# Optimization experiments

Measured on AMD Instinct MI355X. Metric: run time of the kernel, lower is better.

## Reference

```python
import jax, jax.numpy as jnp
import numpy as np
from jax import lax

TOP_K = 8
N_EXPERTS = 256
N_GROUP = 8
TOPK_GROUP = 4
ROUTED_SCALING = 2.5
NORM_TOPK_PROB = True


def setup_inputs() -> dict:
    key = jax.random.key(0)
    k1, k2, k3 = jax.random.split(key, 3)
    hidden_states = jax.random.normal(k1, (4, 4096, 4096), dtype=jnp.float32)
    weight = jax.random.normal(k2, (N_EXPERTS, 4096), dtype=jnp.float32) * 0.02
    e_score_correction_bias = jax.random.normal(k3, (N_EXPERTS,), dtype=jnp.float32) * 0.1
    return {
        "hidden_states": hidden_states,
        "weight": weight,
        "e_score_correction_bias": e_score_correction_bias,
    }


def reference(hidden_states, weight, e_score_correction_bias):
    bsz, seq_len, h = hidden_states.shape
    T = bsz * seq_len
    x = hidden_states.reshape(T, h).astype(jnp.float32)
    # gate GEMM: [T, h] x [E, h]^T -> [T, E]
    logits = jnp.einsum("th,eh->te", x, weight.astype(jnp.float32))
    scores = jax.nn.sigmoid(logits)

    scores_for_choice = scores + e_score_correction_bias[None, :]  # [T, E]
    eg = N_EXPERTS // N_GROUP  # experts per group
    grp = scores_for_choice.reshape(T, N_GROUP, eg)
    top2, _ = lax.top_k(grp, 2)                      # [T, G, 2]
    group_scores = top2.sum(axis=-1)                  # [T, G]
    _, group_idx = lax.top_k(group_scores, TOPK_GROUP)  # [T, topk_group]
    group_mask = jnp.zeros((T, N_GROUP), dtype=scores.dtype)
    group_mask = group_mask.at[jnp.arange(T)[:, None], group_idx].set(1.0)
    score_mask = jnp.broadcast_to(group_mask[:, :, None], (T, N_GROUP, eg)).reshape(T, N_EXPERTS)

    neg_inf = jnp.float32(-jnp.inf)
    tmp_scores = jnp.where(score_mask > 0, scores_for_choice, neg_inf)
    _, topk_idx = lax.top_k(tmp_scores, TOP_K)        # [T, top_k]
    topk_weight = jnp.take_along_axis(scores, topk_idx, axis=1)

    if TOP_K > 1 and NORM_TOPK_PROB:
        denom = topk_weight.sum(axis=-1, keepdims=True) + 1e-20
        topk_weight = topk_weight / denom
    topk_weight = topk_weight * ROUTED_SCALING
    return topk_idx, topk_weight
```

## Files before the change

### kernel.cpp

```cpp
#include <hip/hip_runtime.h>
#include <math.h>

#define Hdim 4096
#define NE 256
#define BM 64
#define BK 32
#define NKC (Hdim / BK)
#define PLANE_ELEMS (Hdim * NE)
#define CHUNK_ELEMS 8192

#define C0 9.765625e-4f
#define C1 4.76837158203125e-7f

typedef _Float16 f16x8 __attribute__((ext_vector_type(8)));
typedef _Float16 f16x4 __attribute__((ext_vector_type(4)));
typedef float f32x4 __attribute__((ext_vector_type(4)));

#define KBAR()                                               \
  {                                                          \
    asm volatile("s_waitcnt lgkmcnt(0)" ::: "memory");       \
    __builtin_amdgcn_s_barrier();                            \
  }

__global__ __launch_bounds__(256)
void convert_w(const float* __restrict__ W, _Float16* __restrict__ pl) {
  const int id = blockIdx.x * 256 + threadIdx.x;
  const int k8 = id & 511;
  const int n = id >> 9;
  const float* src = W + (long)n * Hdim + k8 * 8;
  const float4 x0 = *(const float4*)src;
  const float4 x1 = *(const float4*)(src + 4);
  const float xv[8] = {x0.x, x0.y, x0.z, x0.w, x1.x, x1.y, x1.z, x1.w};
  f16x8 vh, vm;
#pragma unroll
  for (int j = 0; j < 8; ++j) {
    const float v = xv[j] * 64.f;
    const _Float16 h = (_Float16)v;
    const float r = (v - (float)h) * 2048.f;
    vh[j] = h;
    vm[j] = (_Float16)r;
  }
  const long co = ((long)k8 * NE + n) * 8;
  *(f16x8*)(pl + co) = vh;
  *(f16x8*)(pl + PLANE_ELEMS + co) = vm;
}

__global__ __launch_bounds__(512, 2)
void moe_gate_fused(const float* __restrict__ X, const _Float16* __restrict__ pl,
                    const float* __restrict__ bias, float* __restrict__ out, int T) {
  __shared__ __align__(16) unsigned char smem[66560];
  const int tid = threadIdx.x;
  const int lane = tid & 63, wave = tid >> 6;
  const int r16 = lane & 15, c4 = lane >> 4;
  const long bm0 = (long)blockIdx.x * BM;

  f32x4 acc0[4][2], acc1[4][2];
#pragma unroll
  for (int i = 0; i < 4; ++i)
#pragma unroll
    for (int j = 0; j < 2; ++j) {
      acc0[i][j] = (f32x4)(0.f);
      acc1[i][j] = (f32x4)(0.f);
    }

  const int xm = tid >> 3;
  const int f4 = tid & 7;
  const float* xsrc = X + (bm0 + xm) * (long)Hdim + f4 * 4;
  const int k8w = f4 >> 1, hw = f4 & 1;
  const int xws = k8w * 1024 + xm * 16 + hw * 8;

  const _Float16* wsrc0 = pl + ((size_t)(c4 * 256 + wave * 32 + r16)) * 8;
  const _Float16* wsrc1 = wsrc0 + PLANE_ELEMS;

  f16x8 wA[2][2][2], wB[2][2][2];

#define LOADW(dst, pair_)                                                       \
  {                                                                             \
    _Pragma("unroll") for (int sc = 0; sc < 2; ++sc) {                          \
      const size_t ko = (size_t)((pair_) * 2 + sc) * CHUNK_ELEMS;               \
      _Pragma("unroll") for (int fn = 0; fn < 2; ++fn) {                        \
        dst[sc][0][fn] = *(const f16x8*)(wsrc0 + ko + fn * 128);                \
        dst[sc][1][fn] = *(const f16x8*)(wsrc1 + ko + fn * 128);                \
      }                                                                         \
    }                                                                           \
  }

#define LOADX(pair_)                                                            \
  {                                                                             \
    xn0 = *(const float4*)(xsrc + (size_t)(pair_) * 64);                        \
    xn1 = *(const float4*)(xsrc + (size_t)(pair_) * 64 + 32);                   \
  }

#define WRITE_X2(b, xr0, xr1)                                                   \
  {                                                                             \
    _Pragma("unroll") for (int sc = 0; sc < 2; ++sc) {                          \
      const float4 xr = sc ? (xr1) : (xr0);                                     \
      f16x4 vh, vm;                                                             \
      const float xa[4] = {xr.x, xr.y, xr.z, xr.w};                             \
      _Pragma("unroll") for (int j = 0; j < 4; ++j) {                           \
        const float v = xa[j] * 16.f;                                           \
        const _Float16 h = (_Float16)v;                                         \
        const float r = (v - (float)h) * 2048.f;                                \
        vh[j] = h;                                                              \
        vm[j] = (_Float16)r;                                                    \
      }                                                                         \
      const int xo = (b) * 16384 + sc * 8192 + xws;                             \
      *(f16x4*)&smem[xo] = vh;                                                  \
      *(f16x4*)&smem[xo + 4096] = vm;                                           \
    }                                                                           \
  }

#define COMPUTE(b, sc, wreg)                                                    \
  {                                                                             \
    const int xo = (b) * 16384 + (sc) * 8192;                                   \
    f16x8 af[2][4];                                                             \
    _Pragma("unroll") for (int p = 0; p < 2; ++p)                               \
        _Pragma("unroll") for (int fm = 0; fm < 4; ++fm)                        \
            af[p][fm] = *(const f16x8*)&smem[xo + p * 4096 + c4 * 1024 +        \
                                             (fm * 16 + r16) * 16];             \
    _Pragma("unroll") for (int fm = 0; fm < 4; ++fm)                            \
        _Pragma("unroll") for (int fn = 0; fn < 2; ++fn) {                      \
      acc0[fm][fn] = __builtin_amdgcn_mfma_f32_16x16x32_f16(                    \
          af[0][fm], wreg[sc][0][fn], acc0[fm][fn], 0, 0, 0);                   \
      f32x4 s = acc1[fm][fn];                                                   \
      s = __builtin_amdgcn_mfma_f32_16x16x32_f16(af[0][fm], wreg[sc][1][fn], s, 0, 0, 0); \
      s = __builtin_amdgcn_mfma_f32_16x16x32_f16(af[1][fm], wreg[sc][0][fn], s, 0, 0, 0); \
      acc1[fm][fn] = s;                                                         \
    }                                                                           \
  }

  float4 xn0, xn1;

  LOADX(0);
  WRITE_X2(0, xn0, xn1);
  LOADW(wA, 0);
  __syncthreads();

  for (int p = 0; p < NKC / 2; p += 2) {
    {
      LOADX(p + 1);
      LOADW(wB, p + 1);
      __builtin_amdgcn_sched_barrier(0);
      COMPUTE(0, 0, wA);
      COMPUTE(0, 1, wA);
      WRITE_X2(1, xn0, xn1);
      KBAR();
    }
    {
      const int pn = (p + 2 < NKC / 2) ? p + 2 : NKC / 2 - 1;
      LOADX(pn);
      LOADW(wA, pn);
      __builtin_amdgcn_sched_barrier(0);
      COMPUTE(1, 0, wB);
      COMPUTE(1, 1, wB);
      if (p + 2 < NKC / 2) WRITE_X2(0, xn0, xn1);
      KBAR();
    }
  }

  __syncthreads();
  float* lg = (float*)smem;
#pragma unroll
  for (int fm = 0; fm < 4; ++fm)
#pragma unroll
    for (int fn = 0; fn < 2; ++fn)
#pragma unroll
      for (int r = 0; r < 4; ++r) {
        const int t = fm * 16 + c4 * 4 + r;
        const int n = wave * 32 + fn * 16 + r16;
        lg[t * 260 + n] = fmaf(acc1[fm][fn][r], C1, acc0[fm][fn][r] * C0);
      }
  __syncthreads();

  const float4 bv = *(const float4*)(bias + lane * 4);
  for (int i = 0; i < 8; ++i) {
    const int t = wave * 8 + i;
    const float4 lgv = *(const float4*)&lg[t * 260 + lane * 4];

    const float s0 = 1.f / (1.f + expf(-lgv.x));
    const float s1 = 1.f / (1.f + expf(-lgv.y));
    const float s2 = 1.f / (1.f + expf(-lgv.z));
    const float s3 = 1.f / (1.f + expf(-lgv.w));

    const float c0 = s0 + bv.x, c1 = s1 + bv.y, c2 = s2 + bv.z, c3 = s3 + bv.w;

    float m1 = fmaxf(c0, c1), m2 = fminf(c0, c1);
    if (c2 > m1) { m2 = m1; m1 = c2; } else m2 = fmaxf(m2, c2);
    if (c3 > m1) { m2 = m1; m1 = c3; } else m2 = fmaxf(m2, c3);
#pragma unroll
    for (int off = 1; off < 8; off <<= 1) {
      const float o1 = __shfl_xor(m1, off);
      const float o2 = __shfl_xor(m2, off);
      if (o1 > m1) { m2 = fmaxf(m1, o2); m1 = o1; }
      else m2 = fmaxf(m2, o1);
    }
    const float gs = m1 + m2;

    const int gme = lane >> 3;
    int rank = 0;
#pragma unroll
    for (int j = 0; j < 8; ++j) {
      const float gj = __shfl(gs, j * 8);
      rank += ((gj > gs) || (gj == gs && j < gme)) ? 1 : 0;
    }
    const bool sel = rank < 4;

    const float NEG = -INFINITY;
    float q0 = sel ? c0 : NEG, q1 = sel ? c1 : NEG;
    float q2 = sel ? c2 : NEG, q3 = sel ? c3 : NEG;

    float sum = 0.f;
    int my_e = 0;
    float my_w = 0.f;
#pragma unroll
    for (int r = 0; r < 8; ++r) {
      float v = q0; int ix = 0;
      if (q1 > v) { v = q1; ix = 1; }
      if (q2 > v) { v = q2; ix = 2; }
      if (q3 > v) { v = q3; ix = 3; }
      int e = lane * 4 + ix;
#pragma unroll
      for (int off = 1; off < 64; off <<= 1) {
        const float v2 = __shfl_xor(v, off);
        const int e2 = __shfl_xor(e, off);
        const bool take = (v2 > v) || (v2 == v && e2 < e);
        v = take ? v2 : v;
        e = take ? e2 : e;
      }
      const int slot = e & 3, owner = e >> 2;
      const float svs = (slot == 0) ? s0 : ((slot == 1) ? s1 : ((slot == 2) ? s2 : s3));
      const float wgt = __shfl(svs, owner);
      sum += wgt;
      if (lane == r) { my_e = e; my_w = wgt; }
      const bool own = (lane == owner);
      q0 = (own && slot == 0) ? NEG : q0;
      q1 = (own && slot == 1) ? NEG : q1;
      q2 = (own && slot == 2) ? NEG : q2;
      q3 = (own && slot == 3) ? NEG : q3;
    }

    if (lane < 8) {
      const float denom = sum + 1e-20f;
      const long tg = bm0 + t;
      out[tg * 8 + lane] = (float)my_e;
      out[(long)T * 8 + tg * 8 + lane] = my_w / denom * 2.5f;
    }
  }
}

extern "C" void kernel_launch(void* const* d_in, const int* in_sizes, int n_in,
                              void* d_out, int out_size, void* d_ws, size_t ws_size,
                              hipStream_t stream) {
  const float* X = (const float*)d_in[0];
  const float* W = (const float*)d_in[1];
  const float* B = (const float*)d_in[2];
  float* out = (float*)d_out;
  const int T = in_sizes[0] / Hdim;

  _Float16* planes = (_Float16*)d_ws;

  convert_w<<<512, 256, 0, stream>>>(W, planes);
  moe_gate_fused<<<T / BM, 512, 0, stream>>>(X, planes, B, out, T);
}
```

Measured before the change: 155.3 us.

## Split gate GEMM along K into two halves with atomic logit accumulation

The fused GEMM+top-k kernel is split in three: a memset of a logits buffer, a GEMM kernel where each of 512 blocks handles one 64-token tile over half of the K dimension and atomically adds partial logits to global memory, and a separate top-k kernel with one wave per token. This doubles the grid from 256 to 512 blocks to fill more CUs, and shrinks LDS use so occupancy can rise. In exchange it adds a 16 MB logits round trip through global memory, float atomics (order-dependent rounding) and two extra launches.

```diff
diff --git a/kernel.cpp b/kernel.cpp
--- a/kernel.cpp
+++ b/kernel.cpp
@@ -46,13 +46,15 @@
 }
 
 __global__ __launch_bounds__(512, 2)
-void moe_gate_fused(const float* __restrict__ X, const _Float16* __restrict__ pl,
-                    const float* __restrict__ bias, float* __restrict__ out, int T) {
-  __shared__ __align__(16) unsigned char smem[66560];
+void gemm_half(const float* __restrict__ X, const _Float16* __restrict__ pl,
+               float* __restrict__ logits) {
+  __shared__ __align__(16) unsigned char smem[32768];
   const int tid = threadIdx.x;
   const int lane = tid & 63, wave = tid >> 6;
   const int r16 = lane & 15, c4 = lane >> 4;
-  const long bm0 = (long)blockIdx.x * BM;
+  const int tile = blockIdx.x & 255;
+  const int p0 = (blockIdx.x >> 8) * 32;
+  const long bm0 = (long)tile * BM;
 
   f32x4 acc0[4][2], acc1[4][2];
 #pragma unroll
@@ -131,12 +133,12 @@
 
   float4 xn0, xn1;
 
-  LOADX(0);
+  LOADX(p0);
   WRITE_X2(0, xn0, xn1);
-  LOADW(wA, 0);
+  LOADW(wA, p0);
   __syncthreads();
 
-  for (int p = 0; p < NKC / 2; p += 2) {
+  for (int p = p0; p < p0 + 32; p += 2) {
     {
       LOADX(p + 1);
       LOADW(wB, p + 1);
@@ -147,19 +149,17 @@
       KBAR();
     }
     {
-      const int pn = (p + 2 < NKC / 2) ? p + 2 : NKC / 2 - 1;
+      const int pn = (p + 2 < p0 + 32) ? p + 2 : p0 + 31;
       LOADX(pn);
       LOADW(wA, pn);
       __builtin_amdgcn_sched_barrier(0);
       COMPUTE(1, 0, wB);
       COMPUTE(1, 1, wB);
-      if (p + 2 < NKC / 2) WRITE_X2(0, xn0, xn1);
+      if (p + 2 < p0 + 32) WRITE_X2(0, xn0, xn1);
       KBAR();
     }
   }
 
-  __syncthreads();
-  float* lg = (float*)smem;
 #pragma unroll
   for (int fm = 0; fm < 4; ++fm)
 #pragma unroll
@@ -168,83 +168,88 @@
       for (int r = 0; r < 4; ++r) {
         const int t = fm * 16 + c4 * 4 + r;
         const int n = wave * 32 + fn * 16 + r16;
-        lg[t * 260 + n] = fmaf(acc1[fm][fn][r], C1, acc0[fm][fn][r] * C0);
+        atomicAdd(&logits[(bm0 + t) * (long)NE + n],
+                  fmaf(acc1[fm][fn][r], C1, acc0[fm][fn][r] * C0));
       }
-  __syncthreads();
-
+}
+
+__global__ __launch_bounds__(256)
+void moe_gate_topk(const float* __restrict__ logits, const float* __restrict__ bias,
+                   float* __restrict__ out, int T) {
+  const int tid = threadIdx.x;
+  const int lane = tid & 63;
+  const int wv_ = tid >> 6;
+  const int t = blockIdx.x * 4 + wv_;
+
+  const float4 lg = *(const float4*)(logits + (long)t * NE + lane * 4);
   const float4 bv = *(const float4*)(bias + lane * 4);
-  for (int i = 0; i < 8; ++i) {
-    const int t = wave * 8 + i;
-    const float4 lgv = *(const float4*)&lg[t * 260 + lane * 4];
-
-    const float s0 = 1.f / (1.f + expf(-lgv.x));
-    const float s1 = 1.f / (1.f + expf(-lgv.y));
-    const float s2 = 1.f / (1.f + expf(-lgv.z));
-    const float s3 = 1.f / (1.f + expf(-lgv.w));
-
-    const float c0 = s0 + bv.x, c1 = s1 + bv.y, c2 = s2 + bv.z, c3 = s3 + bv.w;
-
-    float m1 = fmaxf(c0, c1), m2 = fminf(c0, c1);
-    if (c2 > m1) { m2 = m1; m1 = c2; } else m2 = fmaxf(m2, c2);
-    if (c3 > m1) { m2 = m1; m1 = c3; } else m2 = fmaxf(m2, c3);
-#pragma unroll
-    for (int off = 1; off < 8; off <<= 1) {
-      const float o1 = __shfl_xor(m1, off);
-      const float o2 = __shfl_xor(m2, off);
-      if (o1 > m1) { m2 = fmaxf(m1, o2); m1 = o1; }
-      else m2 = fmaxf(m2, o1);
-    }
-    const float gs = m1 + m2;
-
-    const int gme = lane >> 3;
-    int rank = 0;
-#pragma unroll
-    for (int j = 0; j < 8; ++j) {
-      const float gj = __shfl(gs, j * 8);
-      rank += ((gj > gs) || (gj == gs && j < gme)) ? 1 : 0;
-    }
-    const bool sel = rank < 4;
-
-    const float NEG = -INFINITY;
-    float q0 = sel ? c0 : NEG, q1 = sel ? c1 : NEG;
-    float q2 = sel ? c2 : NEG, q3 = sel ? c3 : NEG;
-
-    float sum = 0.f;
-    int my_e = 0;
-    float my_w = 0.f;
-#pragma unroll
-    for (int r = 0; r < 8; ++r) {
-      float v = q0; int ix = 0;
-      if (q1 > v) { v = q1; ix = 1; }
-      if (q2 > v) { v = q2; ix = 2; }
-      if (q3 > v) { v = q3; ix = 3; }
-      int e = lane * 4 + ix;
-#pragma unroll
-      for (int off = 1; off < 64; off <<= 1) {
-        const float v2 = __shfl_xor(v, off);
-        const int e2 = __shfl_xor(e, off);
-        const bool take = (v2 > v) || (v2 == v && e2 < e);
-        v = take ? v2 : v;
-        e = take ? e2 : e;
-      }
-      const int slot = e & 3, owner = e >> 2;
-      const float svs = (slot == 0) ? s0 : ((slot == 1) ? s1 : ((slot == 2) ? s2 : s3));
-      const float wgt = __shfl(svs, owner);
-      sum += wgt;
-      if (lane == r) { my_e = e; my_w = wgt; }
-      const bool own = (lane == owner);
-      q0 = (own && slot == 0) ? NEG : q0;
-      q1 = (own && slot == 1) ? NEG : q1;
-      q2 = (own && slot == 2) ? NEG : q2;
-      q3 = (own && slot == 3) ? NEG : q3;
-    }
-
-    if (lane < 8) {
-      const float denom = sum + 1e-20f;
-      const long tg = bm0 + t;
-      out[tg * 8 + lane] = (float)my_e;
-      out[(long)T * 8 + tg * 8 + lane] = my_w / denom * 2.5f;
-    }
+
+  const float s0 = 1.f / (1.f + expf(-lg.x));
+  const float s1 = 1.f / (1.f + expf(-lg.y));
+  const float s2 = 1.f / (1.f + expf(-lg.z));
+  const float s3 = 1.f / (1.f + expf(-lg.w));
+
+  const float c0 = s0 + bv.x, c1 = s1 + bv.y, c2 = s2 + bv.z, c3 = s3 + bv.w;
+
+  float m1 = fmaxf(c0, c1), m2 = fminf(c0, c1);
+  if (c2 > m1) { m2 = m1; m1 = c2; } else m2 = fmaxf(m2, c2);
+  if (c3 > m1) { m2 = m1; m1 = c3; } else m2 = fmaxf(m2, c3);
+#pragma unroll
+  for (int off = 1; off < 8; off <<= 1) {
+    const float o1 = __shfl_xor(m1, off);
+    const float o2 = __shfl_xor(m2, off);
+    if (o1 > m1) { m2 = fmaxf(m1, o2); m1 = o1; }
+    else m2 = fmaxf(m2, o1);
+  }
+  const float gs = m1 + m2;
+
+  const int gme = lane >> 3;
+  int rank = 0;
+#pragma unroll
+  for (int j = 0; j < 8; ++j) {
+    const float gj = __shfl(gs, j * 8);
+    rank += ((gj > gs) || (gj == gs && j < gme)) ? 1 : 0;
+  }
+  const bool sel = rank < 4;
+
+  const float NEG = -INFINITY;
+  float q0 = sel ? c0 : NEG, q1 = sel ? c1 : NEG;
+  float q2 = sel ? c2 : NEG, q3 = sel ? c3 : NEG;
+
+  float sum = 0.f;
+  int my_e = 0;
+  float my_w = 0.f;
+#pragma unroll
+  for (int r = 0; r < 8; ++r) {
+    float v = q0; int ix = 0;
+    if (q1 > v) { v = q1; ix = 1; }
+    if (q2 > v) { v = q2; ix = 2; }
+    if (q3 > v) { v = q3; ix = 3; }
+    int e = lane * 4 + ix;
+#pragma unroll
+    for (int off = 1; off < 64; off <<= 1) {
+      const float v2 = __shfl_xor(v, off);
+      const int e2 = __shfl_xor(e, off);
+      const bool take = (v2 > v) || (v2 == v && e2 < e);
+      v = take ? v2 : v;
+      e = take ? e2 : e;
+    }
+    const int slot = e & 3, owner = e >> 2;
+    const float svs = (slot == 0) ? s0 : ((slot == 1) ? s1 : ((slot == 2) ? s2 : s3));
+    const float wgt = __shfl(svs, owner);
+    sum += wgt;
+    if (lane == r) { my_e = e; my_w = wgt; }
+    const bool own = (lane == owner);
+    q0 = (own && slot == 0) ? NEG : q0;
+    q1 = (own && slot == 1) ? NEG : q1;
+    q2 = (own && slot == 2) ? NEG : q2;
+    q3 = (own && slot == 3) ? NEG : q3;
+  }
+
+  if (lane < 8) {
+    const float denom = sum + 1e-20f;
+    out[(long)t * 8 + lane] = (float)my_e;
+    out[(long)T * 8 + (long)t * 8 + lane] = my_w / denom * 2.5f;
   }
 }
 
@@ -258,7 +263,10 @@
   const int T = in_sizes[0] / Hdim;
 
   _Float16* planes = (_Float16*)d_ws;
+  float* logits = (float*)((char*)d_ws + 4 * 1024 * 1024);
 
   convert_w<<<512, 256, 0, stream>>>(W, planes);
-  moe_gate_fused<<<T / BM, 512, 0, stream>>>(X, planes, B, out, T);
-}
+  hipMemsetAsync(logits, 0, (size_t)T * NE * sizeof(float), stream);
+  gemm_half<<<512, 512, 0, stream>>>(X, planes, logits);
+  moe_gate_topk<<<T / 4, 256, 0, stream>>>(logits, B, out, T);
+}
```

Measured after the change: 167.7 us. 1.08x slower.

## Restructure GEMM mainloop into four-chunk stages with deeper X and W prefetch

Applied to the files above, without the earlier changes.

The k-loop now processes four BK chunks per LDS stage instead of two, halving the number of block barriers. X is prefetched two stages ahead in registers. Weights are double-buffered per chunk, with each next chunk's load issued just before the current chunk's MFMAs. The aim is to cut barrier stalls and better hide global-load latency, at the cost of a larger LDS footprint (doubled X buffers) and more live registers, which may lower occupancy.

```diff
diff --git a/kernel.cpp b/kernel.cpp
--- a/kernel.cpp
+++ b/kernel.cpp
@@ -72,31 +72,29 @@
   const _Float16* wsrc0 = pl + ((size_t)(c4 * 256 + wave * 32 + r16)) * 8;
   const _Float16* wsrc1 = wsrc0 + PLANE_ELEMS;
 
-  f16x8 wA[2][2][2], wB[2][2][2];
-
-#define LOADW(dst, pair_)                                                       \
-  {                                                                             \
-    _Pragma("unroll") for (int sc = 0; sc < 2; ++sc) {                          \
-      const size_t ko = (size_t)((pair_) * 2 + sc) * CHUNK_ELEMS;               \
-      _Pragma("unroll") for (int fn = 0; fn < 2; ++fn) {                        \
-        dst[sc][0][fn] = *(const f16x8*)(wsrc0 + ko + fn * 128);                \
-        dst[sc][1][fn] = *(const f16x8*)(wsrc1 + ko + fn * 128);                \
-      }                                                                         \
-    }                                                                           \
-  }
-
-#define LOADX(pair_)                                                            \
-  {                                                                             \
-    xn0 = *(const float4*)(xsrc + (size_t)(pair_) * 64);                        \
-    xn1 = *(const float4*)(xsrc + (size_t)(pair_) * 64 + 32);                   \
-  }
-
-#define WRITE_X2(b, xr0, xr1)                                                   \
-  {                                                                             \
-    _Pragma("unroll") for (int sc = 0; sc < 2; ++sc) {                          \
-      const float4 xr = sc ? (xr1) : (xr0);                                     \
+  f16x8 wA[2][2], wB[2][2];
+  float4 XA[4], XB[4];
+
+#define LOADW(dst, kc_)                                                         \
+  {                                                                             \
+    const size_t ko = (size_t)(kc_) * CHUNK_ELEMS;                              \
+    _Pragma("unroll") for (int fn = 0; fn < 2; ++fn) {                          \
+      dst[0][fn] = *(const f16x8*)(wsrc0 + ko + fn * 128);                      \
+      dst[1][fn] = *(const f16x8*)(wsrc1 + ko + fn * 128);                      \
+    }                                                                           \
+  }
+
+#define LOADX(dst, q_)                                                          \
+  {                                                                             \
+    _Pragma("unroll") for (int c = 0; c < 4; ++c)                               \
+        dst[c] = *(const float4*)(xsrc + (size_t)(q_) * 128 + c * 32);          \
+  }
+
+#define WRITEX(qb, src_)                                                        \
+  {                                                                             \
+    _Pragma("unroll") for (int c = 0; c < 4; ++c) {                             \
       f16x4 vh, vm;                                                             \
-      const float xa[4] = {xr.x, xr.y, xr.z, xr.w};                             \
+      const float xa[4] = {src_[c].x, src_[c].y, src_[c].z, src_[c].w};         \
       _Pragma("unroll") for (int j = 0; j < 4; ++j) {                           \
         const float v = xa[j] * 16.f;                                           \
         const _Float16 h = (_Float16)v;                                         \
@@ -104,15 +102,15 @@
         vh[j] = h;                                                              \
         vm[j] = (_Float16)r;                                                    \
       }                                                                         \
-      const int xo = (b) * 16384 + sc * 8192 + xws;                             \
+      const int xo = (qb) * 32768 + c * 8192 + xws;                             \
       *(f16x4*)&smem[xo] = vh;                                                  \
       *(f16x4*)&smem[xo + 4096] = vm;                                           \
     }                                                                           \
   }
 
-#define COMPUTE(b, sc, wreg)                                                    \
-  {                                                                             \
-    const int xo = (b) * 16384 + (sc) * 8192;                                   \
+#define COMPUTE(qb, c, wreg)                                                    \
+  {                                                                             \
+    const int xo = (qb) * 32768 + (c) * 8192;                                   \
     f16x8 af[2][4];                                                             \
     _Pragma("unroll") for (int p = 0; p < 2; ++p)                               \
         _Pragma("unroll") for (int fm = 0; fm < 4; ++fm)                        \
@@ -121,41 +119,46 @@
     _Pragma("unroll") for (int fm = 0; fm < 4; ++fm)                            \
         _Pragma("unroll") for (int fn = 0; fn < 2; ++fn) {                      \
       acc0[fm][fn] = __builtin_amdgcn_mfma_f32_16x16x32_f16(                    \
-          af[0][fm], wreg[sc][0][fn], acc0[fm][fn], 0, 0, 0);                   \
+          af[0][fm], wreg[0][fn], acc0[fm][fn], 0, 0, 0);                       \
       f32x4 s = acc1[fm][fn];                                                   \
-      s = __builtin_amdgcn_mfma_f32_16x16x32_f16(af[0][fm], wreg[sc][1][fn], s, 0, 0, 0); \
-      s = __builtin_amdgcn_mfma_f32_16x16x32_f16(af[1][fm], wreg[sc][0][fn], s, 0, 0, 0); \
+      s = __builtin_amdgcn_mfma_f32_16x16x32_f16(af[0][fm], wreg[1][fn], s, 0, 0, 0); \
+      s = __builtin_amdgcn_mfma_f32_16x16x32_f16(af[1][fm], wreg[0][fn], s, 0, 0, 0); \
       acc1[fm][fn] = s;                                                         \
     }                                                                           \
   }
 
-  float4 xn0, xn1;
-
-  LOADX(0);
-  WRITE_X2(0, xn0, xn1);
+#define QUAD(qb, XCUR, XNXT, q_)                                                \
+  {                                                                             \
+    const int qn2 = ((q_) + 2 < 32) ? (q_) + 2 : 31;                            \
+    LOADX(XNXT, qn2);                                                           \
+    LOADW(wB, 4 * (q_) + 1);                                                    \
+    __builtin_amdgcn_sched_barrier(0);                                          \
+    COMPUTE(qb, 0, wA);                                                         \
+    LOADW(wA, 4 * (q_) + 2);                                                    \
+    __builtin_amdgcn_sched_barrier(0);                                          \
+    COMPUTE(qb, 1, wB);                                                         \
+    if ((q_) + 1 < 32) WRITEX((qb) ^ 1, XCUR);                                  \
+    LOADW(wB, 4 * (q_) + 3);                                                    \
+    __builtin_amdgcn_sched_barrier(0);                                          \
+    COMPUTE(qb, 2, wA);                                                         \
+    {                                                                           \
+      const int kcn = (4 * (q_) + 4 < NKC) ? 4 * (q_) + 4 : NKC - 1;            \
+      LOADW(wA, kcn);                                                           \
+    }                                                                           \
+    __builtin_amdgcn_sched_barrier(0);                                          \
+    COMPUTE(qb, 3, wB);                                                         \
+    KBAR();                                                                     \
+  }
+
+  LOADX(XA, 0);
+  WRITEX(0, XA);
+  LOADX(XA, 1);
   LOADW(wA, 0);
   __syncthreads();
 
-  for (int p = 0; p < NKC / 2; p += 2) {
-    {
-      LOADX(p + 1);
-      LOADW(wB, p + 1);
-      __builtin_amdgcn_sched_barrier(0);
-      COMPUTE(0, 0, wA);
-      COMPUTE(0, 1, wA);
-      WRITE_X2(1, xn0, xn1);
-      KBAR();
-    }
-    {
-      const int pn = (p + 2 < NKC / 2) ? p + 2 : NKC / 2 - 1;
-      LOADX(pn);
-      LOADW(wA, pn);
-      __builtin_amdgcn_sched_barrier(0);
-      COMPUTE(1, 0, wB);
-      COMPUTE(1, 1, wB);
-      if (p + 2 < NKC / 2) WRITE_X2(0, xn0, xn1);
-      KBAR();
-    }
+  for (int q = 0; q < 32; q += 2) {
+    QUAD(0, XA, XB, q);
+    QUAD(1, XB, XA, q + 1);
   }
 
   __syncthreads();
```

After: 148.8 us, median of 2. 1.04x faster.
